# Kernel tuning notes

Measured on AMD Instinct MI355X. Metric: run time of the kernel, lower is better.

The kernel has to match this reference:

```python
import jax, jax.numpy as jnp
import numpy as np

N = 50000      # nodes
E = 800000     # edges (avg degree 16)
D = 64         # num_node_features
H = 64         # hidden_channels
G = 512        # graphs in batch
OUT = 32       # final linear output
NEG_SLOPE = 0.2


def setup_inputs() -> dict:
    key = jax.random.key(0)
    ks = jax.random.split(key, 20)
    s = 0.1  # param init scale
    inp = {
        "x": jax.random.normal(ks[0], (N, D), jnp.float32),
        "edge_index": jax.random.randint(ks[1], (2, E), 0, N, dtype=jnp.int64),
        "batch": jnp.sort(jax.random.randint(ks[2], (N,), 0, G, dtype=jnp.int64)),
        # GATv2 layer 1 (D -> H)
        "Wl1": jax.random.normal(ks[3], (D, H), jnp.float32) * s,
        "bl1": jnp.zeros((H,), jnp.float32),
        "Wr1": jax.random.normal(ks[4], (D, H), jnp.float32) * s,
        "br1": jnp.zeros((H,), jnp.float32),
        "att1": jax.random.normal(ks[5], (H,), jnp.float32) * s,
        "bias1": jnp.zeros((H,), jnp.float32),
        # GATv2 layer 2 (H -> H)
        "Wl2": jax.random.normal(ks[6], (H, H), jnp.float32) * s,
        "bl2": jnp.zeros((H,), jnp.float32),
        "Wr2": jax.random.normal(ks[7], (H, H), jnp.float32) * s,
        "br2": jnp.zeros((H,), jnp.float32),
        "att2": jax.random.normal(ks[8], (H,), jnp.float32) * s,
        "bias2": jnp.zeros((H,), jnp.float32),
        # final classifier
        "lin_w": jax.random.normal(ks[9], (H, OUT), jnp.float32) * s,
        "lin_b": jnp.zeros((OUT,), jnp.float32),
    }
    return inp


def _gatv2(x, src, dst, Wl, bl, Wr, br, att, bias):
    # GATv2Conv, heads=1, PyG semantics: messages flow src -> dst
    xl = x @ Wl + bl                       # [N, H] source transform (also the message)
    xr = x @ Wr + br                       # [N, H] destination transform
    z = xl[src] + xr[dst]                  # [E, H] gather
    e = jax.nn.leaky_relu(z, NEG_SLOPE) @ att  # [E] edge scores
    # segment softmax over edges grouped by destination node
    m = jax.ops.segment_max(e, dst, num_segments=N)   # [N]
    ex = jnp.exp(e - m[dst])                          # [E]
    denom = jax.ops.segment_sum(ex, dst, num_segments=N)  # [N]
    alpha = ex / denom[dst]                            # [E]
    out = jax.ops.segment_sum(alpha[:, None] * xl[src], dst, num_segments=N)  # [N, H]
    return out + bias


def reference(x, edge_index, batch,
              Wl1, bl1, Wr1, br1, att1, bias1,
              Wl2, bl2, Wr2, br2, att2, bias2,
              lin_w, lin_b):
    src, dst = edge_index[0], edge_index[1]
    h = jax.nn.relu(_gatv2(x, src, dst, Wl1, bl1, Wr1, br1, att1, bias1))
    h = jax.nn.relu(_gatv2(h, src, dst, Wl2, bl2, Wr2, br2, att2, bias2))
    # global mean pool over graphs
    sums = jax.ops.segment_sum(h, batch, num_segments=G)          # [G, H]
    cnts = jax.ops.segment_sum(jnp.ones((h.shape[0],), h.dtype), batch, num_segments=G)
    pooled = sums / jnp.maximum(cnts, 1.0)[:, None]
    # dropout(p=0.5) is identity at inference
    return pooled @ lin_w + lin_b                                  # [G, 32]
```

## Files before the change

kernel.cpp:

```cpp
#include <hip/hip_runtime.h>
#include <math.h>


#define NEG_BIG (-3.0e38f)
#define ELLC    48
#define OVF_CAP 65536

__global__ __launch_bounds__(256) void ell_fill_kernel(
    const int* __restrict__ src, const int* __restrict__ dst,
    int* __restrict__ cnt, int* __restrict__ ell,
    int* __restrict__ novf, int* __restrict__ ovf_dst, int* __restrict__ ovf_src,
    int E) {
    int e = blockIdx.x * 256 + threadIdx.x;
    if (e >= E) return;
    int d = dst[e];
    int s = src[e];
    int pos = atomicAdd(&cnt[d], 1);
    if (pos < ELLC) {
        __builtin_nontemporal_store(s, &ell[d * ELLC + pos]);
    } else {
        int j = atomicAdd(novf, 1);
        if (j < OVF_CAP) { ovf_dst[j] = d; ovf_src[j] = s; }
    }
}

#define GROWS 32
__global__ __launch_bounds__(256) void dual_gemm64_kernel(
    const float* __restrict__ X,
    const float* __restrict__ Wl, const float* __restrict__ bl,
    const float* __restrict__ Wr, const float* __restrict__ br,
    float* __restrict__ xl, float* __restrict__ xr, int n) {
    __shared__ float WlS[4096], WrS[4096], xS[GROWS * 64];
    int t = threadIdx.x;
    for (int i = t; i < 1024; i += 256) {
        ((float4*)WlS)[i] = ((const float4*)Wl)[i];
        ((float4*)WrS)[i] = ((const float4*)Wr)[i];
    }
    int row0 = blockIdx.x * GROWS;
    for (int i = t; i < GROWS * 16; i += 256) {
        int r = row0 + (i >> 4);
        float4 v = make_float4(0.f, 0.f, 0.f, 0.f);
        if (r < n) v = ((const float4*)(X + (size_t)r * 64))[i & 15];
        ((float4*)xS)[i] = v;
    }
    __syncthreads();
    int h  = t & 63;
    int rb = t >> 6;
    float accl[8], accr[8];
#pragma unroll
    for (int i = 0; i < 8; ++i) { accl[i] = 0.f; accr[i] = 0.f; }
    for (int d = 0; d < 64; ++d) {
        float wl = WlS[d * 64 + h];
        float wr = WrS[d * 64 + h];
#pragma unroll
        for (int i = 0; i < 8; ++i) {
            float xv = xS[(rb + 4 * i) * 64 + d];
            accl[i] += xv * wl;
            accr[i] += xv * wr;
        }
    }
    float blv = bl[h], brv = br[h];
#pragma unroll
    for (int i = 0; i < 8; ++i) {
        int r = row0 + rb + 4 * i;
        if (r < n) {
            xl[(size_t)r * 64 + h] = accl[i] + blv;
            xr[(size_t)r * 64 + h] = accr[i] + brv;
        }
    }
}

__global__ __launch_bounds__(256) void gat_aggregate_kernel(
    const float* __restrict__ xl, const float* __restrict__ xr,
    const int* __restrict__ cnt, const int* __restrict__ ell,
    const int* __restrict__ novf, const int* __restrict__ ovf_dst,
    const int* __restrict__ ovf_src,
    const float* __restrict__ att, const float* __restrict__ bias,
    float* __restrict__ out, int n) {
    int wid  = (blockIdx.x * blockDim.x + threadIdx.x) >> 6;
    int lane = threadIdx.x & 63;
    if (wid >= n) return;
    int g = lane >> 4;
    int l = lane & 15;
    int d = wid;

    float4 xr4  = ((const float4*)(xr + (size_t)d * 64))[l];
    float4 att4 = ((const float4*)att)[l];
    int deg_d = cnt[d];
    int beg = d * ELLC;
    int end = beg + min(deg_d, ELLC);

    float  m = NEG_BIG, s = 0.f;
    float4 acc = make_float4(0.f, 0.f, 0.f, 0.f);
    int p = beg;

    for (; p + 8 <= end; p += 8) {
        int i0 = ell[p + g];
        int i1 = ell[p + 4 + g];
        float4 x0 = ((const float4*)(xl + (size_t)i0 * 64))[l];
        float4 x1 = ((const float4*)(xl + (size_t)i1 * 64))[l];
        float z, c0 = 0.f, c1 = 0.f;
        z = x0.x + xr4.x; c0 += ((z > 0.f) ? z : 0.2f * z) * att4.x;
        z = x0.y + xr4.y; c0 += ((z > 0.f) ? z : 0.2f * z) * att4.y;
        z = x0.z + xr4.z; c0 += ((z > 0.f) ? z : 0.2f * z) * att4.z;
        z = x0.w + xr4.w; c0 += ((z > 0.f) ? z : 0.2f * z) * att4.w;
        z = x1.x + xr4.x; c1 += ((z > 0.f) ? z : 0.2f * z) * att4.x;
        z = x1.y + xr4.y; c1 += ((z > 0.f) ? z : 0.2f * z) * att4.y;
        z = x1.z + xr4.z; c1 += ((z > 0.f) ? z : 0.2f * z) * att4.z;
        z = x1.w + xr4.w; c1 += ((z > 0.f) ? z : 0.2f * z) * att4.w;
#pragma unroll
        for (int sh = 8; sh >= 1; sh >>= 1) {
            c0 += __shfl_xor(c0, sh);
            c1 += __shfl_xor(c1, sh);
        }
        float mn = fmaxf(m, fmaxf(c0, c1));
        float ra = __expf(m - mn);
        float p0 = __expf(c0 - mn);
        float p1 = __expf(c1 - mn);
        s = s * ra + p0 + p1;
        acc.x = acc.x * ra + p0 * x0.x + p1 * x1.x;
        acc.y = acc.y * ra + p0 * x0.y + p1 * x1.y;
        acc.z = acc.z * ra + p0 * x0.z + p1 * x1.z;
        acc.w = acc.w * ra + p0 * x0.w + p1 * x1.w;
        m = mn;
    }
    for (; p < end; p += 4) {
        int  e      = p + g;
        bool active = (e < end);
        int  i0     = active ? ell[e] : 0;
        float4 x0 = ((const float4*)(xl + (size_t)i0 * 64))[l];
        float z, c0 = 0.f;
        z = x0.x + xr4.x; c0 += ((z > 0.f) ? z : 0.2f * z) * att4.x;
        z = x0.y + xr4.y; c0 += ((z > 0.f) ? z : 0.2f * z) * att4.y;
        z = x0.z + xr4.z; c0 += ((z > 0.f) ? z : 0.2f * z) * att4.z;
        z = x0.w + xr4.w; c0 += ((z > 0.f) ? z : 0.2f * z) * att4.w;
#pragma unroll
        for (int sh = 8; sh >= 1; sh >>= 1) c0 += __shfl_xor(c0, sh);
        if (!active) c0 = -INFINITY;
        float mn = fmaxf(m, c0);
        float ra = __expf(m - mn);
        float cb = __expf(c0 - mn);
        s = s * ra + cb;
        acc.x = acc.x * ra + cb * x0.x;
        acc.y = acc.y * ra + cb * x0.y;
        acc.z = acc.z * ra + cb * x0.z;
        acc.w = acc.w * ra + cb * x0.w;
        m = mn;
    }
    if (deg_d > ELLC) {
        int no = min(*novf, OVF_CAP);
        for (int j = g; j < no; j += 4) {
            bool active = (ovf_dst[j] == d);
            int  i0     = active ? ovf_src[j] : 0;
            float4 x0 = ((const float4*)(xl + (size_t)i0 * 64))[l];
            float z, c0 = 0.f;
            z = x0.x + xr4.x; c0 += ((z > 0.f) ? z : 0.2f * z) * att4.x;
            z = x0.y + xr4.y; c0 += ((z > 0.f) ? z : 0.2f * z) * att4.y;
            z = x0.z + xr4.z; c0 += ((z > 0.f) ? z : 0.2f * z) * att4.z;
            z = x0.w + xr4.w; c0 += ((z > 0.f) ? z : 0.2f * z) * att4.w;
#pragma unroll
            for (int sh = 8; sh >= 1; sh >>= 1) c0 += __shfl_xor(c0, sh);
            if (!active) c0 = -INFINITY;
            float mn = fmaxf(m, c0);
            float ra = __expf(m - mn);
            float cb = __expf(c0 - mn);
            s = s * ra + cb;
            acc.x = acc.x * ra + cb * x0.x;
            acc.y = acc.y * ra + cb * x0.y;
            acc.z = acc.z * ra + cb * x0.z;
            acc.w = acc.w * ra + cb * x0.w;
            m = mn;
        }
    }
#pragma unroll
    for (int mask = 16; mask <= 32; mask <<= 1) {
        float mo = __shfl_xor(m, mask);
        float so = __shfl_xor(s, mask);
        float ax = __shfl_xor(acc.x, mask);
        float ay = __shfl_xor(acc.y, mask);
        float az = __shfl_xor(acc.z, mask);
        float aw = __shfl_xor(acc.w, mask);
        float mn = fmaxf(m, mo);
        float ra = __expf(m - mn);
        float rb = __expf(mo - mn);
        s = s * ra + so * rb;
        acc.x = acc.x * ra + ax * rb;
        acc.y = acc.y * ra + ay * rb;
        acc.z = acc.z * ra + az * rb;
        acc.w = acc.w * ra + aw * rb;
        m = mn;
    }
    if (g == 0) {
        float inv = (s > 0.f) ? (1.f / s) : 0.f;
        float4 b4 = ((const float4*)bias)[l];
        float4 v;
        v.x = fmaxf(acc.x * inv + b4.x, 0.f);
        v.y = fmaxf(acc.y * inv + b4.y, 0.f);
        v.z = fmaxf(acc.z * inv + b4.z, 0.f);
        v.w = fmaxf(acc.w * inv + b4.w, 0.f);
        ((float4*)(out + (size_t)d * 64))[l] = v;
    }
}

__global__ __launch_bounds__(256) void pool_kernel(
    const float* __restrict__ h, const int* __restrict__ batch,
    float* __restrict__ sums, float* __restrict__ cnts, int n, int nwaves) {
    int wid  = (blockIdx.x * blockDim.x + threadIdx.x) >> 6;
    int lane = threadIdx.x & 63;
    int per   = (n + nwaves - 1) / nwaves;
    int start = wid * per;
    int end   = min(n, start + per);
    if (start >= end) return;
    int cur   = batch[start];
    float acc = 0.f, cnt = 0.f;
    for (int i = start; i < end; ++i) {
        int g = batch[i];
        if (g != cur) {
            atomicAdd(&sums[cur * 64 + lane], acc);
            if (lane == 0) atomicAdd(&cnts[cur], cnt);
            acc = 0.f; cnt = 0.f; cur = g;
        }
        acc += h[(size_t)i * 64 + lane];
        cnt += 1.f;
    }
    atomicAdd(&sums[cur * 64 + lane], acc);
    if (lane == 0) atomicAdd(&cnts[cur], cnt);
}

__global__ __launch_bounds__(256) void final_kernel(
    const float* __restrict__ sums, const float* __restrict__ cnts,
    const float* __restrict__ lin_w, const float* __restrict__ lin_b,
    float* __restrict__ out, int total) {
    int tid = blockIdx.x * blockDim.x + threadIdx.x;
    if (tid >= total) return;
    int g = tid >> 5, o = tid & 31;
    float inv = 1.f / fmaxf(cnts[g], 1.f);
    float a = 0.f;
    for (int h = 0; h < 64; ++h) a += sums[g * 64 + h] * lin_w[h * 32 + o];
    out[tid] = a * inv + lin_b[o];
}

extern "C" void kernel_launch(void* const* d_in, const int* in_sizes, int n_in,
                              void* d_out, int out_size, void* d_ws, size_t ws_size,
                              hipStream_t stream) {
    const float* x     = (const float*)d_in[0];
    const int*   ei    = (const int*)d_in[1];
    const int*   batch = (const int*)d_in[2];
    const float* Wl1   = (const float*)d_in[3];
    const float* bl1   = (const float*)d_in[4];
    const float* Wr1   = (const float*)d_in[5];
    const float* br1   = (const float*)d_in[6];
    const float* att1  = (const float*)d_in[7];
    const float* bias1 = (const float*)d_in[8];
    const float* Wl2   = (const float*)d_in[9];
    const float* bl2   = (const float*)d_in[10];
    const float* Wr2   = (const float*)d_in[11];
    const float* br2   = (const float*)d_in[12];
    const float* att2  = (const float*)d_in[13];
    const float* bias2 = (const float*)d_in[14];
    const float* lin_w = (const float*)d_in[15];
    const float* lin_b = (const float*)d_in[16];
    float* out = (float*)d_out;

    const int N = in_sizes[0] / 64;
    const int E = in_sizes[1] / 2;
    const int G = out_size / 32;
    const int* src = ei;
    const int* dst = ei + E;

    char*  ws  = (char*)d_ws;
    size_t off = 0;
    auto alloc = [&](size_t bytes) -> void* {
        void* p = ws + off;
        off += bytes;
        off = (off + 255) & ~(size_t)255;
        return p;
    };
    float* xl      = (float*)alloc((size_t)N * 64 * sizeof(float));
    float* xr      = (float*)alloc((size_t)N * 64 * sizeof(float));
    float* h1      = (float*)alloc((size_t)N * 64 * sizeof(float));
    int*   cnt     = (int*)alloc((size_t)N * sizeof(int));
    int*   novf    = (int*)alloc(256);
    float* sums    = (float*)alloc((size_t)G * 64 * sizeof(float));
    float* cnts    = (float*)alloc((size_t)G * sizeof(float));
    char*  zend    = ws + off;
    int*   ell     = (int*)alloc((size_t)N * ELLC * sizeof(int));
    int*   ovf_dst = (int*)alloc((size_t)OVF_CAP * sizeof(int));
    int*   ovf_src = (int*)alloc((size_t)OVF_CAP * sizeof(int));

    hipMemsetAsync(cnt, 0, (size_t)(zend - (char*)cnt), stream);

    int egrid = (E + 255) / 256;
    int ggrid = (N + GROWS - 1) / GROWS;
    int agrid = (N + 3) / 4;

    ell_fill_kernel<<<egrid, 256, 0, stream>>>(src, dst, cnt, ell,
                                               novf, ovf_dst, ovf_src, E);

    dual_gemm64_kernel<<<ggrid, 256, 0, stream>>>(x, Wl1, bl1, Wr1, br1, xl, xr, N);
    gat_aggregate_kernel<<<agrid, 256, 0, stream>>>(
        xl, xr, cnt, ell, novf, ovf_dst, ovf_src, att1, bias1, h1, N);

    dual_gemm64_kernel<<<ggrid, 256, 0, stream>>>(h1, Wl2, bl2, Wr2, br2, xl, xr, N);
    gat_aggregate_kernel<<<agrid, 256, 0, stream>>>(
        xl, xr, cnt, ell, novf, ovf_dst, ovf_src, att2, bias2, h1, N);

    const int NWAVES = 1024;
    pool_kernel<<<256, 256, 0, stream>>>(h1, batch, sums, cnts, N, NWAVES);
    int total = G * 32;
    final_kernel<<<(total + 255) / 256, 256, 0, stream>>>(sums, cnts, lin_w, lin_b, out, total);
}
```

Before: 289.2 us.

## Replace global-atomic ELL fill with per-block destination-range scan using shared-memory counters

Result: slower. 542.6 us (+87.6%).

```diff
diff --git a/kernel.cpp b/kernel.cpp
--- a/kernel.cpp
+++ b/kernel.cpp
@@ -5,23 +5,55 @@
 #define NEG_BIG (-3.0e38f)
 #define ELLC    48
 #define OVF_CAP 65536
-
-__global__ __launch_bounds__(256) void ell_fill_kernel(
+#define FILL_B  256
+
+__global__ __launch_bounds__(256) void scan_fill_kernel(
     const int* __restrict__ src, const int* __restrict__ dst,
     int* __restrict__ cnt, int* __restrict__ ell,
     int* __restrict__ novf, int* __restrict__ ovf_dst, int* __restrict__ ovf_src,
-    int E) {
-    int e = blockIdx.x * 256 + threadIdx.x;
-    if (e >= E) return;
-    int d = dst[e];
-    int s = src[e];
-    int pos = atomicAdd(&cnt[d], 1);
-    if (pos < ELLC) {
-        __builtin_nontemporal_store(s, &ell[d * ELLC + pos]);
-    } else {
-        int j = atomicAdd(novf, 1);
-        if (j < OVF_CAP) { ovf_dst[j] = d; ovf_src[j] = s; }
-    }
+    int E, int N, int nodes_per_blk) {
+    __shared__ int lcnt[256];
+    int t  = threadIdx.x;
+    int d0 = blockIdx.x * nodes_per_blk;
+    int d1 = min(N, d0 + nodes_per_blk);
+    lcnt[t] = 0;
+    __syncthreads();
+
+    const int4* dst4 = (const int4*)dst;
+    int nq = E >> 2;
+    for (int q = t; q < nq; q += 256) {
+        int4 dv = dst4[q];
+        int e = q << 2;
+#pragma unroll
+        for (int k = 0; k < 4; ++k) {
+            int d = (k == 0) ? dv.x : (k == 1) ? dv.y : (k == 2) ? dv.z : dv.w;
+            if (d >= d0 && d < d1) {
+                int pos = atomicAdd(&lcnt[d - d0], 1);
+                int s   = src[e + k];
+                if (pos < ELLC) {
+                    ell[d * ELLC + pos] = s;
+                } else {
+                    int j = atomicAdd(novf, 1);
+                    if (j < OVF_CAP) { ovf_dst[j] = d; ovf_src[j] = s; }
+                }
+            }
+        }
+    }
+    for (int e = (nq << 2) + t; e < E; e += 256) {
+        int d = dst[e];
+        if (d >= d0 && d < d1) {
+            int pos = atomicAdd(&lcnt[d - d0], 1);
+            int s   = src[e];
+            if (pos < ELLC) {
+                ell[d * ELLC + pos] = s;
+            } else {
+                int j = atomicAdd(novf, 1);
+                if (j < OVF_CAP) { ovf_dst[j] = d; ovf_src[j] = s; }
+            }
+        }
+    }
+    __syncthreads();
+    if (d0 + t < d1) cnt[d0 + t] = lcnt[t];
 }
 
 #define GROWS 32
@@ -279,23 +311,23 @@
     float* xl      = (float*)alloc((size_t)N * 64 * sizeof(float));
     float* xr      = (float*)alloc((size_t)N * 64 * sizeof(float));
     float* h1      = (float*)alloc((size_t)N * 64 * sizeof(float));
-    int*   cnt     = (int*)alloc((size_t)N * sizeof(int));
     int*   novf    = (int*)alloc(256);
     float* sums    = (float*)alloc((size_t)G * 64 * sizeof(float));
     float* cnts    = (float*)alloc((size_t)G * sizeof(float));
     char*  zend    = ws + off;
+    int*   cnt     = (int*)alloc((size_t)N * sizeof(int));
     int*   ell     = (int*)alloc((size_t)N * ELLC * sizeof(int));
     int*   ovf_dst = (int*)alloc((size_t)OVF_CAP * sizeof(int));
     int*   ovf_src = (int*)alloc((size_t)OVF_CAP * sizeof(int));
 
-    hipMemsetAsync(cnt, 0, (size_t)(zend - (char*)cnt), stream);
-
-    int egrid = (E + 255) / 256;
+    hipMemsetAsync(novf, 0, (size_t)(zend - (char*)novf), stream);
+
     int ggrid = (N + GROWS - 1) / GROWS;
     int agrid = (N + 3) / 4;
-
-    ell_fill_kernel<<<egrid, 256, 0, stream>>>(src, dst, cnt, ell,
-                                               novf, ovf_dst, ovf_src, E);
+    int npb   = (N + FILL_B - 1) / FILL_B;
+
+    scan_fill_kernel<<<FILL_B, 256, 0, stream>>>(
+        src, dst, cnt, ell, novf, ovf_dst, ovf_src, E, N, npb);
 
     dual_gemm64_kernel<<<ggrid, 256, 0, stream>>>(x, Wl1, bl1, Wr1, br1, xl, xr, N);
     gat_aggregate_kernel<<<agrid, 256, 0, stream>>>(
```
